# Kernel optimization log

Hardware: AMD Instinct MI355X
Metric: run time of the kernel (lower is better)

## Reference

```python
import jax, jax.numpy as jnp
import numpy as np

INPUT_DIM = 1024
EMBED_DIM = 1024
NUM_HEADS = 16
HEAD_DIM = EMBED_DIM // NUM_HEADS


def setup_inputs() -> dict:
    key = jax.random.key(0)
    k_x, k_qkv, k_w, k_b = jax.random.split(key, 4)
    B, N = 2, 2048
    x = jax.random.normal(k_x, (B, N, INPUT_DIM), dtype=jnp.float32)
    # nn.Linear weights: stored [out, in]; scale like torch default init
    s1 = 1.0 / np.sqrt(INPUT_DIM)
    s2 = 1.0 / np.sqrt(EMBED_DIM)
    W_qkv = jax.random.uniform(k_qkv, (3 * EMBED_DIM, INPUT_DIM), jnp.float32, -s1, s1)
    W_out = jax.random.uniform(k_w, (EMBED_DIM, EMBED_DIM), jnp.float32, -s2, s2)
    b_out = jax.random.uniform(k_b, (EMBED_DIM,), jnp.float32, -s2, s2)
    return {"x": x, "W_qkv": W_qkv, "W_out": W_out, "b_out": b_out}


def reference(x, W_qkv, W_out, b_out):
    B, N, C = x.shape
    # qkv projection (no bias): [B, N, 3*embed]
    qkv = jnp.einsum('bnc,ec->bne', x, W_qkv)
    q = qkv[:, :, 0:EMBED_DIM].reshape(B, N, NUM_HEADS, HEAD_DIM)
    k = qkv[:, :, EMBED_DIM:2 * EMBED_DIM].reshape(B, N, NUM_HEADS, HEAD_DIM)
    v = qkv[:, :, 2 * EMBED_DIM:3 * EMBED_DIM].reshape(B, N, NUM_HEADS, HEAD_DIM)
    scores = jnp.einsum('bihd,bjhd->bhij', q, k) / jnp.sqrt(jnp.float32(HEAD_DIM))
    attn = jax.nn.softmax(scores, axis=-1)
    out = jnp.einsum('bhij,bjhd->bihd', attn, v).reshape(B, N, EMBED_DIM)
    return jnp.einsum('bne,oe->bno', out, W_out) + b_out
```

## Files before the change

### kernel.cpp

```cpp
#include <hip/hip_runtime.h>
#include <stdint.h>

typedef __attribute__((ext_vector_type(8))) short short8;
typedef __attribute__((ext_vector_type(4))) short bf16x4;
typedef __attribute__((ext_vector_type(4))) float f32x4;

#define MFMA32(a, b, c) __builtin_amdgcn_mfma_f32_16x16x32_bf16((a), (b), (c), 0, 0, 0)
#define MFMA16(a, b, c) __builtin_amdgcn_mfma_f32_16x16x16bf16_1k((a), (b), (c), 0, 0, 0)

__device__ __forceinline__ uint16_t f32_to_bf16(float f) {
  union { float f; uint32_t u; } v; v.f = f;
  uint32_t u = v.u;
  u += 0x7FFFu + ((u >> 16) & 1u);
  return (uint16_t)(u >> 16);
}
__device__ __forceinline__ uint16_t f32_to_bf16_fast(float f) {
  union { float f; uint32_t u; } v; v.f = f;
  return (uint16_t)((v.u + 0x8000u) >> 16);
}

__device__ __forceinline__ void load_lds16(const uint16_t* g, uint16_t* l) {
  __builtin_amdgcn_global_load_lds(
      (const __attribute__((address_space(1))) uint32_t*)g,
      (__attribute__((address_space(3))) uint32_t*)l, 16, 0, 0);
}

__global__ __launch_bounds__(256) void cvt3_kernel(
    const float* __restrict__ x, const float* __restrict__ w1,
    const float* __restrict__ w2, uint16_t* __restrict__ xb,
    uint16_t* __restrict__ w1b, uint16_t* __restrict__ w2b) {
  const int i = blockIdx.x * 256 + threadIdx.x;
  const float4* src;
  ushort4* dst;
  int off;
  if (i < 1048576) { src = (const float4*)x;  dst = (ushort4*)xb;  off = i; }
  else if (i < 1835008) { src = (const float4*)w1; dst = (ushort4*)w1b; off = i - 1048576; }
  else { src = (const float4*)w2; dst = (ushort4*)w2b; off = i - 1835008; }
  const float4 v = src[off];
  ushort4 o;
  o.x = f32_to_bf16(v.x);
  o.y = f32_to_bf16(v.y);
  o.z = f32_to_bf16(v.z);
  o.w = f32_to_bf16(v.w);
  dst[off] = o;
}

template <int MODE>
__global__ __launch_bounds__(256) void gemm_abt_kernel(
    const uint16_t* __restrict__ A, const uint16_t* __restrict__ Bt,
    float* __restrict__ Cf, const float* __restrict__ bias,
    uint16_t* __restrict__ Qh, uint16_t* __restrict__ Kh, uint16_t* __restrict__ Vh,
    int M, int N, int K) {
  __shared__ __align__(16) uint16_t As[128 * 32];
  __shared__ __align__(16) uint16_t Bs[128 * 32];
  const int tid = threadIdx.x;
  const int wave = tid >> 6;
  const int lane = tid & 63;
  const int quad = lane >> 4;
  const int l16 = lane & 15;
  const int row0 = blockIdx.x * 128;
  const int col0 = blockIdx.y * 128;
  const int wm = (wave >> 1) * 64;
  const int wn = (wave & 1) * 64;

  f32x4 acc[4][4];
#pragma unroll
  for (int a = 0; a < 4; ++a)
#pragma unroll
    for (int b = 0; b < 4; ++b) acc[a][b] = (f32x4){0.f, 0.f, 0.f, 0.f};

  const uint16_t* gA = A + (size_t)(row0 + wave * 32 + (lane >> 2)) * K + (lane & 3) * 8;
  const uint16_t* gB = Bt + (size_t)(col0 + wave * 32 + (lane >> 2)) * K + (lane & 3) * 8;
  uint16_t* lA = As + wave * 1024;
  uint16_t* lB = Bs + wave * 1024;

  for (int k0 = 0; k0 < K; k0 += 32) {
    load_lds16(gA, lA);
    load_lds16(gA + (size_t)16 * K, lA + 512);
    load_lds16(gB, lB);
    load_lds16(gB + (size_t)16 * K, lB + 512);
    gA += 32;
    gB += 32;
    __syncthreads();
    short8 af[4], bf[4];
#pragma unroll
    for (int mt = 0; mt < 4; ++mt)
      af[mt] = *(const short8*)&As[(wm + mt * 16 + l16) * 32 + quad * 8];
#pragma unroll
    for (int nt = 0; nt < 4; ++nt)
      bf[nt] = *(const short8*)&Bs[(wn + nt * 16 + l16) * 32 + quad * 8];
#pragma unroll
    for (int mt = 0; mt < 4; ++mt)
#pragma unroll
      for (int nt = 0; nt < 4; ++nt)
        acc[mt][nt] = MFMA32(af[mt], bf[nt], acc[mt][nt]);
    __syncthreads();
  }

#pragma unroll
  for (int mt = 0; mt < 4; ++mt) {
#pragma unroll
    for (int nt = 0; nt < 4; ++nt) {
      const int col = col0 + wn + nt * 16 + l16;
#pragma unroll
      for (int r = 0; r < 4; ++r) {
        const int row = row0 + wm + mt * 16 + quad * 4 + r;
        const float val = acc[mt][nt][r];
        if constexpr (MODE == 0) {
          Cf[(size_t)row * N + col] = val + bias[col];
        } else {
          const int which = col >> 10;
          const int hc = (col & 1023) >> 6;
          const int d = col & 63;
          const int b = row >> 11;
          const int nn = row & 2047;
          const size_t hb = (size_t)(b * 16 + hc) * 131072;
          if (which == 0) {
            Qh[hb + (size_t)nn * 64 + d] = f32_to_bf16(val * 0.1803368801111244f);
          } else if (which == 1) {
            const uint16_t bv = f32_to_bf16(val);
            const int jt = nn >> 6, st = (nn >> 4) & 3, j16 = nn & 15;
            const int kc = d >> 5, qd = (d >> 3) & 3, e = d & 7;
            Kh[hb + jt * 4096 + st * 1024 + kc * 512 + (qd * 16 + j16) * 8 + e] = bv;
          } else {
            const uint16_t bv = f32_to_bf16(val);
            const int jt = nn >> 6, j = nn & 63;
            const int st = j >> 4, qv = (j >> 2) & 3, e = j & 3;
            const int tt = d >> 4, d16 = d & 15;
            Vh[hb + jt * 4096 + ((st * 2 + (tt >> 1)) * 64 + qv * 16 + d16) * 8 +
               (tt & 1) * 4 + e] = bv;
          }
        }
      }
    }
  }
}

__global__ __launch_bounds__(256, 2) void attn_kernel(
    const uint16_t* __restrict__ Qh, const uint16_t* __restrict__ Kh,
    const uint16_t* __restrict__ Vh, uint16_t* __restrict__ out) {
  __shared__ __align__(16) uint16_t Ks[2][4096];
  __shared__ __align__(16) uint16_t Vs[2][4096];
  const int tid = threadIdx.x;
  const int wave = tid >> 6;
  const int lane = tid & 63;
  const int quad = lane >> 4;
  const int l16 = lane & 15;
  const int bx = blockIdx.x;
  const int it = bx & 15;
  const int h = (bx >> 4) & 15;
  const int ib = bx >> 8;
  const int i0 = it * 128 + wave * 32;
  const size_t hb = (size_t)(ib * 16 + h) * 131072;

  short8 qf[2][2];
#pragma unroll
  for (int m = 0; m < 2; ++m)
#pragma unroll
    for (int kc = 0; kc < 2; ++kc)
      qf[m][kc] = *(const short8*)(Qh + hb + (size_t)(i0 + m * 16 + l16) * 64 + kc * 32 + quad * 8);

  f32x4 o[2][4], o4[2];
#pragma unroll
  for (int m = 0; m < 2; ++m) {
    o4[m] = (f32x4){0.f, 0.f, 0.f, 0.f};
#pragma unroll
    for (int t = 0; t < 4; ++t) o[m][t] = (f32x4){0.f, 0.f, 0.f, 0.f};
  }

  const bf16x4 ones4 = {(short)0x3F80, (short)0x3F80, (short)0x3F80, (short)0x3F80};

  const uint16_t* gK = Kh + hb + wave * 1024 + lane * 8;
  const uint16_t* gV = Vh + hb + wave * 1024 + lane * 8;
  const int so = wave * 1024;

  load_lds16(gK, &Ks[0][so]);
  load_lds16(gK + 512, &Ks[0][so + 512]);
  load_lds16(gV, &Vs[0][so]);
  load_lds16(gV + 512, &Vs[0][so + 512]);
  __syncthreads();

#pragma unroll 2
  for (int t = 0; t < 32; ++t) {
    const int cur = t & 1;
    if (t < 31) {
      const size_t goff = (size_t)(t + 1) * 4096;
      load_lds16(gK + goff, &Ks[cur ^ 1][so]);
      load_lds16(gK + goff + 512, &Ks[cur ^ 1][so + 512]);
      load_lds16(gV + goff, &Vs[cur ^ 1][so]);
      load_lds16(gV + goff + 512, &Vs[cur ^ 1][so + 512]);
    }

    short8 kf[8];
#pragma unroll
    for (int i = 0; i < 8; ++i) kf[i] = *(const short8*)&Ks[cur][i * 512 + lane * 8];

    f32x4 s[2][4];
#pragma unroll
    for (int m = 0; m < 2; ++m)
#pragma unroll
      for (int st = 0; st < 4; ++st) {
        f32x4 sc = (f32x4){0.f, 0.f, 0.f, 0.f};
        sc = MFMA32(kf[st * 2 + 0], qf[m][0], sc);
        sc = MFMA32(kf[st * 2 + 1], qf[m][1], sc);
        s[m][st] = sc;
      }

    short8 v8[8];
#pragma unroll
    for (int i = 0; i < 8; ++i) v8[i] = *(const short8*)&Vs[cur][i * 512 + lane * 8];

    bf16x4 p4[2][4];
#pragma unroll
    for (int m = 0; m < 2; ++m)
#pragma unroll
      for (int st = 0; st < 4; ++st) {
        bf16x4 p;
#pragma unroll
        for (int r = 0; r < 4; ++r)
          p[r] = (short)f32_to_bf16_fast(__builtin_amdgcn_exp2f(s[m][st][r]));
        p4[m][st] = p;
      }

#pragma unroll
    for (int st = 0; st < 4; ++st) {
#pragma unroll
      for (int m = 0; m < 2; ++m) {
        o4[m] = MFMA16(p4[m][st], ones4, o4[m]);
#pragma unroll
        for (int tth = 0; tth < 2; ++tth) {
          const short8 w = v8[st * 2 + tth];
          const bf16x4 vlo = {w[0], w[1], w[2], w[3]};
          const bf16x4 vhi = {w[4], w[5], w[6], w[7]};
          o[m][tth * 2 + 0] = MFMA16(p4[m][st], vlo, o[m][tth * 2 + 0]);
          o[m][tth * 2 + 1] = MFMA16(p4[m][st], vhi, o[m][tth * 2 + 1]);
        }
      }
    }

    __syncthreads();
  }

#pragma unroll
  for (int m = 0; m < 2; ++m)
#pragma unroll
    for (int r = 0; r < 4; ++r) {
      const float inv = 1.0f / o4[m][r];
      const int row = i0 + m * 16 + quad * 4 + r;
      const size_t obase = (size_t)(ib * 2048 + row) * 1024 + h * 64;
#pragma unroll
      for (int tt = 0; tt < 4; ++tt)
        out[obase + tt * 16 + l16] = f32_to_bf16(o[m][tt][r] * inv);
    }
}

extern "C" void kernel_launch(void* const* d_in, const int* in_sizes, int n_in,
                              void* d_out, int out_size, void* d_ws, size_t ws_size,
                              hipStream_t stream) {
  const float* x = (const float*)d_in[0];
  const float* Wqkv = (const float*)d_in[1];
  const float* Wout = (const float*)d_in[2];
  const float* bout = (const float*)d_in[3];

  uint16_t* xb = (uint16_t*)d_ws;
  uint16_t* wqkvb = xb + (size_t)4096 * 1024;
  uint16_t* woutb = wqkvb + (size_t)3072 * 1024;
  uint16_t* qh = woutb + (size_t)1024 * 1024;
  uint16_t* kh = qh + (size_t)32 * 131072;
  uint16_t* vh = kh + (size_t)32 * 131072;
  uint16_t* attnb = vh + (size_t)32 * 131072;

  cvt3_kernel<<<8192, 256, 0, stream>>>(x, Wqkv, Wout, xb, wqkvb, woutb);

  dim3 g1(4096 / 128, 3072 / 128);
  gemm_abt_kernel<1><<<g1, dim3(256), 0, stream>>>(
      xb, wqkvb, nullptr, nullptr, qh, kh, vh, 4096, 3072, 1024);

  attn_kernel<<<512, 256, 0, stream>>>(qh, kh, vh, attnb);

  dim3 g2(4096 / 128, 1024 / 128);
  gemm_abt_kernel<0><<<g2, dim3(256), 0, stream>>>(
      attnb, woutb, (float*)d_out, bout, nullptr, nullptr, nullptr, 4096, 1024, 1024);
}
```

Measured before the change: 194.2 us.

## Add 256x256 double-buffered QKV GEMM kernel with interleaved async LDS loads

Replaces the templated 128x128 GEMM used for the QKV projection with a dedicated 512-thread kernel. It uses 256x256 tiles, a K-step of 64 and double-buffered LDS filled by direct global-to-LDS loads. Loads for the next K tile are interleaved with MFMA phases, and wave priority is raised around the MFMA bursts, to overlap memory with compute and reuse more data per LDS load. In exchange it launches only 192 blocks, fewer than the CU count, and each block holds a large LDS footprint. The unpadded LDS layout may also cause bank conflicts. The output GEMM is kept as a plain non-templated kernel.

```diff
diff --git a/kernel.cpp b/kernel.cpp
--- a/kernel.cpp
+++ b/kernel.cpp
@@ -45,12 +45,9 @@
   dst[off] = o;
 }
 
-template <int MODE>
 __global__ __launch_bounds__(256) void gemm_abt_kernel(
     const uint16_t* __restrict__ A, const uint16_t* __restrict__ Bt,
-    float* __restrict__ Cf, const float* __restrict__ bias,
-    uint16_t* __restrict__ Qh, uint16_t* __restrict__ Kh, uint16_t* __restrict__ Vh,
-    int M, int N, int K) {
+    float* __restrict__ Cf, const float* __restrict__ bias, int M, int N, int K) {
   __shared__ __align__(16) uint16_t As[128 * 32];
   __shared__ __align__(16) uint16_t Bs[128 * 32];
   const int tid = threadIdx.x;
@@ -105,31 +102,116 @@
 #pragma unroll
       for (int r = 0; r < 4; ++r) {
         const int row = row0 + wm + mt * 16 + quad * 4 + r;
+        Cf[(size_t)row * N + col] = acc[mt][nt][r] + bias[col];
+      }
+    }
+  }
+}
+
+__global__ __launch_bounds__(512, 2) void gemm_qkv256_kernel(
+    const uint16_t* __restrict__ A, const uint16_t* __restrict__ Bt,
+    uint16_t* __restrict__ Qh, uint16_t* __restrict__ Kh, uint16_t* __restrict__ Vh) {
+  __shared__ __align__(16) uint16_t As[2][256 * 64];
+  __shared__ __align__(16) uint16_t Bs[2][256 * 64];
+  const int tid = threadIdx.x;
+  const int wave = tid >> 6;
+  const int lane = tid & 63;
+  const int quad = lane >> 4;
+  const int l16 = lane & 15;
+  const int wr = wave >> 2;
+  const int wc = wave & 3;
+  const int row0 = blockIdx.x * 256;
+  const int col0 = blockIdx.y * 256;
+  const int K = 1024;
+
+  f32x4 acc[8][4];
+#pragma unroll
+  for (int a = 0; a < 8; ++a)
+#pragma unroll
+    for (int b = 0; b < 4; ++b) acc[a][b] = (f32x4){0.f, 0.f, 0.f, 0.f};
+
+  const uint16_t* gA = A + (size_t)(row0 + wave * 8 + (lane >> 3)) * K + (lane & 7) * 8;
+  const uint16_t* gB = Bt + (size_t)(col0 + wave * 8 + (lane >> 3)) * K + (lane & 7) * 8;
+  const int ldsw = wave * 512;
+
+#define STAGE2(buf, t, s)                                                      \
+  do {                                                                         \
+    load_lds16(gA + (size_t)(s) * 64 * K + (t) * 64, &As[buf][(s)*4096 + ldsw]); \
+    load_lds16(gB + (size_t)(s) * 64 * K + (t) * 64, &Bs[buf][(s)*4096 + ldsw]); \
+  } while (0)
+
+  short8 bfr[4];
+
+#define PHASE(buf, q, ks, readB)                                               \
+  do {                                                                         \
+    short8 af[4];                                                              \
+    _Pragma("unroll") for (int i = 0; i < 4; ++i)                              \
+        af[i] = *(const short8*)&As[buf][(wr * 128 + ((q)*4 + i) * 16 + l16) * 64 + (ks)*32 + quad * 8]; \
+    if (readB) {                                                               \
+      _Pragma("unroll") for (int n = 0; n < 4; ++n)                            \
+          bfr[n] = *(const short8*)&Bs[buf][(wc * 64 + n * 16 + l16) * 64 + (ks)*32 + quad * 8]; \
+    }                                                                          \
+    __builtin_amdgcn_s_setprio(1);                                             \
+    _Pragma("unroll") for (int i = 0; i < 4; ++i)                              \
+        _Pragma("unroll") for (int n = 0; n < 4; ++n)                          \
+            acc[(q)*4 + i][n] = MFMA32(af[i], bfr[n], acc[(q)*4 + i][n]);      \
+    __builtin_amdgcn_s_setprio(0);                                             \
+  } while (0)
+
+#pragma unroll
+  for (int s = 0; s < 4; ++s) STAGE2(0, 0, s);
+  __syncthreads();
+
+  for (int j = 0; j < 8; ++j) {
+    const int t1 = 2 * j + 1;
+    STAGE2(1, t1, 0); PHASE(0, 0, 0, 1);
+    STAGE2(1, t1, 1); PHASE(0, 1, 0, 0);
+    STAGE2(1, t1, 2); PHASE(0, 0, 1, 1);
+    STAGE2(1, t1, 3); PHASE(0, 1, 1, 0);
+    __syncthreads();
+    if (j < 7) {
+      const int t2 = 2 * j + 2;
+      STAGE2(0, t2, 0); PHASE(1, 0, 0, 1);
+      STAGE2(0, t2, 1); PHASE(1, 1, 0, 0);
+      STAGE2(0, t2, 2); PHASE(1, 0, 1, 1);
+      STAGE2(0, t2, 3); PHASE(1, 1, 1, 0);
+    } else {
+      PHASE(1, 0, 0, 1); PHASE(1, 1, 0, 0); PHASE(1, 0, 1, 1); PHASE(1, 1, 1, 0);
+    }
+    __syncthreads();
+  }
+#undef STAGE2
+#undef PHASE
+
+#pragma unroll
+  for (int mt = 0; mt < 8; ++mt) {
+#pragma unroll
+    for (int nt = 0; nt < 4; ++nt) {
+      const int col = col0 + wc * 64 + nt * 16 + l16;
+      const int which = col >> 10;
+      const int hc = (col & 1023) >> 6;
+      const int d = col & 63;
+#pragma unroll
+      for (int r = 0; r < 4; ++r) {
+        const int row = row0 + wr * 128 + mt * 16 + quad * 4 + r;
         const float val = acc[mt][nt][r];
-        if constexpr (MODE == 0) {
-          Cf[(size_t)row * N + col] = val + bias[col];
+        const int b = row >> 11;
+        const int nn = row & 2047;
+        const size_t hb = (size_t)(b * 16 + hc) * 131072;
+        if (which == 0) {
+          Qh[hb + (size_t)nn * 64 + d] = f32_to_bf16(val * 0.1803368801111244f);
+        } else if (which == 1) {
+          const uint16_t bv = f32_to_bf16(val);
+          const int jt = nn >> 6, st = (nn >> 4) & 3, j16 = nn & 15;
+          const int kc = d >> 5, qd = (d >> 3) & 3, e = d & 7;
+          Kh[hb + jt * 4096 + st * 1024 + kc * 512 + (qd * 16 + j16) * 8 + e] = bv;
         } else {
-          const int which = col >> 10;
-          const int hc = (col & 1023) >> 6;
-          const int d = col & 63;
-          const int b = row >> 11;
-          const int nn = row & 2047;
-          const size_t hb = (size_t)(b * 16 + hc) * 131072;
-          if (which == 0) {
-            Qh[hb + (size_t)nn * 64 + d] = f32_to_bf16(val * 0.1803368801111244f);
-          } else if (which == 1) {
-            const uint16_t bv = f32_to_bf16(val);
-            const int jt = nn >> 6, st = (nn >> 4) & 3, j16 = nn & 15;
-            const int kc = d >> 5, qd = (d >> 3) & 3, e = d & 7;
-            Kh[hb + jt * 4096 + st * 1024 + kc * 512 + (qd * 16 + j16) * 8 + e] = bv;
-          } else {
-            const uint16_t bv = f32_to_bf16(val);
-            const int jt = nn >> 6, j = nn & 63;
-            const int st = j >> 4, qv = (j >> 2) & 3, e = j & 3;
-            const int tt = d >> 4, d16 = d & 15;
-            Vh[hb + jt * 4096 + ((st * 2 + (tt >> 1)) * 64 + qv * 16 + d16) * 8 +
-               (tt & 1) * 4 + e] = bv;
-          }
+          const uint16_t bv = f32_to_bf16(val);
+          const int jt = nn >> 6, j = nn & 63;
+          const int st = j >> 4, qv = (j >> 2) & 3, e = j & 3;
+          const int tt = d >> 4, d16 = d & 15;
+          Vh[hb + jt * 4096 + ((st * 2 + (tt >> 1)) * 64 + qv * 16 + d16) * 8 +
+             (tt & 1) * 4 + e] = bv;
         }
       }
     }
@@ -272,13 +354,12 @@
 
   cvt3_kernel<<<8192, 256, 0, stream>>>(x, Wqkv, Wout, xb, wqkvb, woutb);
 
-  dim3 g1(4096 / 128, 3072 / 128);
-  gemm_abt_kernel<1><<<g1, dim3(256), 0, stream>>>(
-      xb, wqkvb, nullptr, nullptr, qh, kh, vh, 4096, 3072, 1024);
+  gemm_qkv256_kernel<<<dim3(4096 / 256, 3072 / 256), 512, 0, stream>>>(
+      xb, wqkvb, qh, kh, vh);
 
   attn_kernel<<<512, 256, 0, stream>>>(qh, kh, vh, attnb);
 
   dim3 g2(4096 / 128, 1024 / 128);
-  gemm_abt_kernel<0><<<g2, dim3(256), 0, stream>>>(
-      attnb, woutb, (float*)d_out, bout, nullptr, nullptr, nullptr, 4096, 1024, 1024);
-}
+  gemm_abt_kernel<<<g2, dim3(256), 0, stream>>>(
+      attnb, woutb, (float*)d_out, bout, 4096, 1024, 1024);
+}
```

Result: slower. 212.1 us (+9.2%).

## Add dedicated QKV GEMM with 256x128 tiles, triple-buffered async LDS loads and swizzling

Applied to the files above, without the earlier changes.

The QKV projection moves from the generic templated GEMM into a new kernel. It uses 512 threads, a 256x128 output tile, BK=64 and a three-stage LDS ring filled by global_load_lds with an XOR swizzle to avoid bank conflicts. MFMA sections are bracketed with s_setprio, and the scattered Q/K/V head-layout epilogue is kept. The goal is to overlap global loads with MFMA work and raise arithmetic intensity per block. The cost is about 147KB of LDS, so only one block fits per CU. The fixed vmcnt(12) wait does not drain fully in the last two iterations, which risks a race on the tail stages.

```diff
diff --git a/kernel.cpp b/kernel.cpp
--- a/kernel.cpp
+++ b/kernel.cpp
@@ -45,12 +45,9 @@
   dst[off] = o;
 }
 
-template <int MODE>
 __global__ __launch_bounds__(256) void gemm_abt_kernel(
     const uint16_t* __restrict__ A, const uint16_t* __restrict__ Bt,
-    float* __restrict__ Cf, const float* __restrict__ bias,
-    uint16_t* __restrict__ Qh, uint16_t* __restrict__ Kh, uint16_t* __restrict__ Vh,
-    int M, int N, int K) {
+    float* __restrict__ Cf, const float* __restrict__ bias, int M, int N, int K) {
   __shared__ __align__(16) uint16_t As[128 * 32];
   __shared__ __align__(16) uint16_t Bs[128 * 32];
   const int tid = threadIdx.x;
@@ -105,31 +102,118 @@
 #pragma unroll
       for (int r = 0; r < 4; ++r) {
         const int row = row0 + wm + mt * 16 + quad * 4 + r;
+        Cf[(size_t)row * N + col] = acc[mt][nt][r] + bias[col];
+      }
+    }
+  }
+}
+
+__global__ __launch_bounds__(512, 2) void gemm_qkv_kernel(
+    const uint16_t* __restrict__ A, const uint16_t* __restrict__ Bt,
+    uint16_t* __restrict__ Qh, uint16_t* __restrict__ Kh, uint16_t* __restrict__ Vh) {
+  __shared__ __align__(16) uint16_t As3[3][256 * 64];
+  __shared__ __align__(16) uint16_t Bs3[3][128 * 64];
+  const int tid = threadIdx.x;
+  const int wave = tid >> 6;
+  const int lane = tid & 63;
+  const int quad = lane >> 4;
+  const int l16 = lane & 15;
+  const int wr = wave >> 2;
+  const int wc = wave & 3;
+  const int row0 = blockIdx.x * 256;
+  const int col0 = blockIdx.y * 128;
+  const int K = 1024;
+
+  f32x4 acc[8][2];
+#pragma unroll
+  for (int a = 0; a < 8; ++a)
+#pragma unroll
+    for (int b = 0; b < 2; ++b) acc[a][b] = (f32x4){0.f, 0.f, 0.f, 0.f};
+
+  const int swz8 = ((lane & 7) ^ ((lane >> 3) & 7)) * 8;
+  const uint16_t* gA = A + (size_t)(row0 + wave * 8 + (lane >> 3)) * K + swz8;
+  const uint16_t* gB = Bt + (size_t)(col0 + wave * 8 + (lane >> 3)) * K + swz8;
+  const int ldsw = wave * 512;
+
+#define STAGEA(slot, t, s) \
+  load_lds16(gA + (size_t)(s) * 64 * K + (size_t)(t) * 64, &As3[slot][(s) * 4096 + ldsw])
+#define STAGEB(slot, t, s) \
+  load_lds16(gB + (size_t)(s) * 64 * K + (size_t)(t) * 64, &Bs3[slot][(s) * 4096 + ldsw])
+#define STAGE6(slot, t)                                          \
+  do {                                                           \
+    STAGEA(slot, t, 0); STAGEA(slot, t, 1);                      \
+    STAGEA(slot, t, 2); STAGEA(slot, t, 3);                      \
+    STAGEB(slot, t, 0); STAGEB(slot, t, 1);                      \
+  } while (0)
+
+  STAGE6(0, 0);
+  STAGE6(1, 1);
+  STAGE6(2, 2);
+
+  for (int t = 0; t < 16; ++t) {
+    const int st = t % 3;
+    asm volatile("s_waitcnt vmcnt(12)" ::: "memory");
+    __builtin_amdgcn_s_barrier();
+
+    const uint16_t* as = As3[st];
+    const uint16_t* bs = Bs3[st];
+#pragma unroll
+    for (int ks = 0; ks < 2; ++ks) {
+      const int cswz = (((ks * 4 + quad) ^ (l16 & 7)) * 8);
+      const short8 b0 = *(const short8*)&bs[(wc * 32 + l16) * 64 + cswz];
+      const short8 b1 = *(const short8*)&bs[(wc * 32 + 16 + l16) * 64 + cswz];
+#pragma unroll
+      for (int mq = 0; mq < 2; ++mq) {
+        short8 af[4];
+#pragma unroll
+        for (int i = 0; i < 4; ++i)
+          af[i] = *(const short8*)&as[(wr * 128 + (mq * 4 + i) * 16 + l16) * 64 + cswz];
+        __builtin_amdgcn_s_setprio(1);
+#pragma unroll
+        for (int i = 0; i < 4; ++i) {
+          acc[mq * 4 + i][0] = MFMA32(af[i], b0, acc[mq * 4 + i][0]);
+          acc[mq * 4 + i][1] = MFMA32(af[i], b1, acc[mq * 4 + i][1]);
+        }
+        __builtin_amdgcn_s_setprio(0);
+      }
+    }
+
+    __builtin_amdgcn_s_barrier();
+    if (t + 3 < 16) STAGE6(st, t + 3);
+  }
+#undef STAGEA
+#undef STAGEB
+#undef STAGE6
+
+#pragma unroll
+  for (int mt = 0; mt < 8; ++mt) {
+#pragma unroll
+    for (int nt = 0; nt < 2; ++nt) {
+      const int col = col0 + wc * 32 + nt * 16 + l16;
+      const int which = col >> 10;
+      const int hc = (col & 1023) >> 6;
+      const int d = col & 63;
+#pragma unroll
+      for (int r = 0; r < 4; ++r) {
+        const int row = row0 + wr * 128 + mt * 16 + quad * 4 + r;
         const float val = acc[mt][nt][r];
-        if constexpr (MODE == 0) {
-          Cf[(size_t)row * N + col] = val + bias[col];
+        const int b = row >> 11;
+        const int nn = row & 2047;
+        const size_t hb = (size_t)(b * 16 + hc) * 131072;
+        if (which == 0) {
+          Qh[hb + (size_t)nn * 64 + d] = f32_to_bf16(val * 0.1803368801111244f);
+        } else if (which == 1) {
+          const uint16_t bv = f32_to_bf16(val);
+          const int jt = nn >> 6, st2 = (nn >> 4) & 3, j16 = nn & 15;
+          const int kc = d >> 5, qd = (d >> 3) & 3, e = d & 7;
+          Kh[hb + jt * 4096 + st2 * 1024 + kc * 512 + (qd * 16 + j16) * 8 + e] = bv;
         } else {
-          const int which = col >> 10;
-          const int hc = (col & 1023) >> 6;
-          const int d = col & 63;
-          const int b = row >> 11;
-          const int nn = row & 2047;
-          const size_t hb = (size_t)(b * 16 + hc) * 131072;
-          if (which == 0) {
-            Qh[hb + (size_t)nn * 64 + d] = f32_to_bf16(val * 0.1803368801111244f);
-          } else if (which == 1) {
-            const uint16_t bv = f32_to_bf16(val);
-            const int jt = nn >> 6, st = (nn >> 4) & 3, j16 = nn & 15;
-            const int kc = d >> 5, qd = (d >> 3) & 3, e = d & 7;
-            Kh[hb + jt * 4096 + st * 1024 + kc * 512 + (qd * 16 + j16) * 8 + e] = bv;
-          } else {
-            const uint16_t bv = f32_to_bf16(val);
-            const int jt = nn >> 6, j = nn & 63;
-            const int st = j >> 4, qv = (j >> 2) & 3, e = j & 3;
-            const int tt = d >> 4, d16 = d & 15;
-            Vh[hb + jt * 4096 + ((st * 2 + (tt >> 1)) * 64 + qv * 16 + d16) * 8 +
-               (tt & 1) * 4 + e] = bv;
-          }
+          const uint16_t bv = f32_to_bf16(val);
+          const int jt = nn >> 6, j = nn & 63;
+          const int st2 = j >> 4, qv = (j >> 2) & 3, e = j & 3;
+          const int tt = d >> 4, d16 = d & 15;
+          Vh[hb + jt * 4096 + ((st2 * 2 + (tt >> 1)) * 64 + qv * 16 + d16) * 8 +
+             (tt & 1) * 4 + e] = bv;
         }
       }
     }
@@ -272,13 +356,12 @@
 
   cvt3_kernel<<<8192, 256, 0, stream>>>(x, Wqkv, Wout, xb, wqkvb, woutb);
 
-  dim3 g1(4096 / 128, 3072 / 128);
-  gemm_abt_kernel<1><<<g1, dim3(256), 0, stream>>>(
-      xb, wqkvb, nullptr, nullptr, qh, kh, vh, 4096, 3072, 1024);
+  gemm_qkv_kernel<<<dim3(4096 / 256, 3072 / 128), 512, 0, stream>>>(
+      xb, wqkvb, qh, kh, vh);
 
   attn_kernel<<<512, 256, 0, stream>>>(qh, kh, vh, attnb);
 
   dim3 g2(4096 / 128, 1024 / 128);
-  gemm_abt_kernel<0><<<g2, dim3(256), 0, stream>>>(
-      attnb, woutb, (float*)d_out, bout, nullptr, nullptr, nullptr, 4096, 1024, 1024);
-}
+  gemm_abt_kernel<<<g2, dim3(256), 0, stream>>>(
+      attnb, woutb, (float*)d_out, bout, 4096, 1024, 1024);
+}
```

New measurement: 206.3 us. 6.2% more time.

## Use BK=64 XOR-swizzled LDS tiles and narrower output-projection GEMM tiles

Applied to the files above, without the earlier changes.

Both GEMMs now stage 64-wide K slices in LDS with an XOR swizzle on the 16-byte chunk index, which halves the number of barrier pairs per K loop and avoids LDS bank conflicts on fragment reads. The templated GEMM is split into a QKV-specialized kernel and an output-projection kernel with hard-coded sizes. The output GEMM uses 128x64 tiles, doubling its grid to 512 blocks for better CU occupancy, at the cost of re-reading A more often.

```diff
diff --git a/kernel.cpp b/kernel.cpp
--- a/kernel.cpp
+++ b/kernel.cpp
@@ -45,14 +45,11 @@
   dst[off] = o;
 }
 
-template <int MODE>
-__global__ __launch_bounds__(256) void gemm_abt_kernel(
+__global__ __launch_bounds__(256) void gemm_qkv_kernel(
     const uint16_t* __restrict__ A, const uint16_t* __restrict__ Bt,
-    float* __restrict__ Cf, const float* __restrict__ bias,
-    uint16_t* __restrict__ Qh, uint16_t* __restrict__ Kh, uint16_t* __restrict__ Vh,
-    int M, int N, int K) {
-  __shared__ __align__(16) uint16_t As[128 * 32];
-  __shared__ __align__(16) uint16_t Bs[128 * 32];
+    uint16_t* __restrict__ Qh, uint16_t* __restrict__ Kh, uint16_t* __restrict__ Vh) {
+  __shared__ __align__(16) uint16_t As[128 * 64];
+  __shared__ __align__(16) uint16_t Bs[128 * 64];
   const int tid = threadIdx.x;
   const int wave = tid >> 6;
   const int lane = tid & 63;
@@ -62,6 +59,7 @@
   const int col0 = blockIdx.y * 128;
   const int wm = (wave >> 1) * 64;
   const int wn = (wave & 1) * 64;
+  const int K = 1024;
 
   f32x4 acc[4][4];
 #pragma unroll
@@ -69,31 +67,33 @@
 #pragma unroll
     for (int b = 0; b < 4; ++b) acc[a][b] = (f32x4){0.f, 0.f, 0.f, 0.f};
 
-  const uint16_t* gA = A + (size_t)(row0 + wave * 32 + (lane >> 2)) * K + (lane & 3) * 8;
-  const uint16_t* gB = Bt + (size_t)(col0 + wave * 32 + (lane >> 2)) * K + (lane & 3) * 8;
-  uint16_t* lA = As + wave * 1024;
-  uint16_t* lB = Bs + wave * 1024;
-
-  for (int k0 = 0; k0 < K; k0 += 32) {
-    load_lds16(gA, lA);
-    load_lds16(gA + (size_t)16 * K, lA + 512);
-    load_lds16(gB, lB);
-    load_lds16(gB + (size_t)16 * K, lB + 512);
-    gA += 32;
-    gB += 32;
-    __syncthreads();
-    short8 af[4], bf[4];
-#pragma unroll
-    for (int mt = 0; mt < 4; ++mt)
-      af[mt] = *(const short8*)&As[(wm + mt * 16 + l16) * 32 + quad * 8];
-#pragma unroll
-    for (int nt = 0; nt < 4; ++nt)
-      bf[nt] = *(const short8*)&Bs[(wn + nt * 16 + l16) * 32 + quad * 8];
-#pragma unroll
-    for (int mt = 0; mt < 4; ++mt)
+  const int swz8 = ((lane & 7) ^ ((lane >> 3) & 7)) * 8;
+  const uint16_t* gA = A + (size_t)(row0 + wave * 32 + (lane >> 3)) * K + swz8;
+  const uint16_t* gB = Bt + (size_t)(col0 + wave * 32 + (lane >> 3)) * K + swz8;
+
+  for (int k0 = 0; k0 < K; k0 += 64) {
+#pragma unroll
+    for (int s = 0; s < 4; ++s) {
+      load_lds16(gA + (size_t)s * 8 * K + k0, &As[(wave * 32 + s * 8) * 64]);
+      load_lds16(gB + (size_t)s * 8 * K + k0, &Bs[(wave * 32 + s * 8) * 64]);
+    }
+    __syncthreads();
+#pragma unroll
+    for (int ks = 0; ks < 2; ++ks) {
+      const int cswz = (((ks * 4 + quad) ^ (l16 & 7)) * 8);
+      short8 af[4], bf[4];
+#pragma unroll
+      for (int mt = 0; mt < 4; ++mt)
+        af[mt] = *(const short8*)&As[(wm + mt * 16 + l16) * 64 + cswz];
 #pragma unroll
       for (int nt = 0; nt < 4; ++nt)
-        acc[mt][nt] = MFMA32(af[mt], bf[nt], acc[mt][nt]);
+        bf[nt] = *(const short8*)&Bs[(wn + nt * 16 + l16) * 64 + cswz];
+#pragma unroll
+      for (int mt = 0; mt < 4; ++mt)
+#pragma unroll
+        for (int nt = 0; nt < 4; ++nt)
+          acc[mt][nt] = MFMA32(af[mt], bf[nt], acc[mt][nt]);
+    }
     __syncthreads();
   }
 
@@ -102,35 +102,99 @@
 #pragma unroll
     for (int nt = 0; nt < 4; ++nt) {
       const int col = col0 + wn + nt * 16 + l16;
+      const int which = col >> 10;
+      const int hc = (col & 1023) >> 6;
+      const int d = col & 63;
 #pragma unroll
       for (int r = 0; r < 4; ++r) {
         const int row = row0 + wm + mt * 16 + quad * 4 + r;
         const float val = acc[mt][nt][r];
-        if constexpr (MODE == 0) {
-          Cf[(size_t)row * N + col] = val + bias[col];
+        const int b = row >> 11;
+        const int nn = row & 2047;
+        const size_t hb = (size_t)(b * 16 + hc) * 131072;
+        if (which == 0) {
+          Qh[hb + (size_t)nn * 64 + d] = f32_to_bf16(val * 0.1803368801111244f);
+        } else if (which == 1) {
+          const uint16_t bv = f32_to_bf16(val);
+          const int jt = nn >> 6, st = (nn >> 4) & 3, j16 = nn & 15;
+          const int kc = d >> 5, qd = (d >> 3) & 3, e = d & 7;
+          Kh[hb + jt * 4096 + st * 1024 + kc * 512 + (qd * 16 + j16) * 8 + e] = bv;
         } else {
-          const int which = col >> 10;
-          const int hc = (col & 1023) >> 6;
-          const int d = col & 63;
-          const int b = row >> 11;
-          const int nn = row & 2047;
-          const size_t hb = (size_t)(b * 16 + hc) * 131072;
-          if (which == 0) {
-            Qh[hb + (size_t)nn * 64 + d] = f32_to_bf16(val * 0.1803368801111244f);
-          } else if (which == 1) {
-            const uint16_t bv = f32_to_bf16(val);
-            const int jt = nn >> 6, st = (nn >> 4) & 3, j16 = nn & 15;
-            const int kc = d >> 5, qd = (d >> 3) & 3, e = d & 7;
-            Kh[hb + jt * 4096 + st * 1024 + kc * 512 + (qd * 16 + j16) * 8 + e] = bv;
-          } else {
-            const uint16_t bv = f32_to_bf16(val);
-            const int jt = nn >> 6, j = nn & 63;
-            const int st = j >> 4, qv = (j >> 2) & 3, e = j & 3;
-            const int tt = d >> 4, d16 = d & 15;
-            Vh[hb + jt * 4096 + ((st * 2 + (tt >> 1)) * 64 + qv * 16 + d16) * 8 +
-               (tt & 1) * 4 + e] = bv;
-          }
+          const uint16_t bv = f32_to_bf16(val);
+          const int jt = nn >> 6, j = nn & 63;
+          const int st = j >> 4, qv = (j >> 2) & 3, e = j & 3;
+          const int tt = d >> 4, d16 = d & 15;
+          Vh[hb + jt * 4096 + ((st * 2 + (tt >> 1)) * 64 + qv * 16 + d16) * 8 +
+             (tt & 1) * 4 + e] = bv;
         }
+      }
+    }
+  }
+}
+
+__global__ __launch_bounds__(256) void gemm_out_kernel(
+    const uint16_t* __restrict__ A, const uint16_t* __restrict__ Bt,
+    float* __restrict__ Cf, const float* __restrict__ bias) {
+  __shared__ __align__(16) uint16_t As[128 * 64];
+  __shared__ __align__(16) uint16_t Bs[64 * 64];
+  const int tid = threadIdx.x;
+  const int wave = tid >> 6;
+  const int lane = tid & 63;
+  const int quad = lane >> 4;
+  const int l16 = lane & 15;
+  const int row0 = blockIdx.x * 128;
+  const int col0 = blockIdx.y * 64;
+  const int wm = (wave >> 1) * 64;
+  const int wn = (wave & 1) * 32;
+  const int K = 1024;
+  const int N = 1024;
+
+  f32x4 acc[4][2];
+#pragma unroll
+  for (int a = 0; a < 4; ++a)
+#pragma unroll
+    for (int b = 0; b < 2; ++b) acc[a][b] = (f32x4){0.f, 0.f, 0.f, 0.f};
+
+  const int swz8 = ((lane & 7) ^ ((lane >> 3) & 7)) * 8;
+  const uint16_t* gA = A + (size_t)(row0 + wave * 32 + (lane >> 3)) * K + swz8;
+  const uint16_t* gB = Bt + (size_t)(col0 + wave * 16 + (lane >> 3)) * K + swz8;
+
+  for (int k0 = 0; k0 < K; k0 += 64) {
+#pragma unroll
+    for (int s = 0; s < 4; ++s)
+      load_lds16(gA + (size_t)s * 8 * K + k0, &As[(wave * 32 + s * 8) * 64]);
+#pragma unroll
+    for (int s = 0; s < 2; ++s)
+      load_lds16(gB + (size_t)s * 8 * K + k0, &Bs[(wave * 16 + s * 8) * 64]);
+    __syncthreads();
+#pragma unroll
+    for (int ks = 0; ks < 2; ++ks) {
+      const int cswz = (((ks * 4 + quad) ^ (l16 & 7)) * 8);
+      short8 af[4], bf[2];
+#pragma unroll
+      for (int mt = 0; mt < 4; ++mt)
+        af[mt] = *(const short8*)&As[(wm + mt * 16 + l16) * 64 + cswz];
+#pragma unroll
+      for (int nt = 0; nt < 2; ++nt)
+        bf[nt] = *(const short8*)&Bs[(wn + nt * 16 + l16) * 64 + cswz];
+#pragma unroll
+      for (int mt = 0; mt < 4; ++mt)
+#pragma unroll
+        for (int nt = 0; nt < 2; ++nt)
+          acc[mt][nt] = MFMA32(af[mt], bf[nt], acc[mt][nt]);
+    }
+    __syncthreads();
+  }
+
+#pragma unroll
+  for (int mt = 0; mt < 4; ++mt) {
+#pragma unroll
+    for (int nt = 0; nt < 2; ++nt) {
+      const int col = col0 + wn + nt * 16 + l16;
+#pragma unroll
+      for (int r = 0; r < 4; ++r) {
+        const int row = row0 + wm + mt * 16 + quad * 4 + r;
+        Cf[(size_t)row * N + col] = acc[mt][nt][r] + bias[col];
       }
     }
   }
@@ -272,13 +336,11 @@
 
   cvt3_kernel<<<8192, 256, 0, stream>>>(x, Wqkv, Wout, xb, wqkvb, woutb);
 
-  dim3 g1(4096 / 128, 3072 / 128);
-  gemm_abt_kernel<1><<<g1, dim3(256), 0, stream>>>(
-      xb, wqkvb, nullptr, nullptr, qh, kh, vh, 4096, 3072, 1024);
+  gemm_qkv_kernel<<<dim3(4096 / 128, 3072 / 128), 256, 0, stream>>>(
+      xb, wqkvb, qh, kh, vh);
 
   attn_kernel<<<512, 256, 0, stream>>>(qh, kh, vh, attnb);
 
-  dim3 g2(4096 / 128, 1024 / 128);
-  gemm_abt_kernel<0><<<g2, dim3(256), 0, stream>>>(
-      attnb, woutb, (float*)d_out, bout, nullptr, nullptr, nullptr, 4096, 1024, 1024);
-}
+  gemm_out_kernel<<<dim3(4096 / 128, 1024 / 64), 256, 0, stream>>>(
+      attnb, woutb, (float*)d_out, bout);
+}
```

Result: faster. 185.0 us (-4.8%).
